# Kernel tuning notes

Hardware: AMD Instinct MI355X
Metric: run time of the kernel (lower is better)

The kernel has to match this reference:

```python
import jax, jax.numpy as jnp
import numpy as np

B, L, D = 4, 1024, 1024
N, H = 16, 64
FFW = 4096
LYR = 6
PDIM = 768            # 3 * 16^2
POS_EMB = 64
POOL_K = 4
EPS = 1e-6
BASE = 10000.0
GRID = 32             # 32x32 patch grid


def rms_norm(x, scale=None, eps=EPS):
    v = jnp.mean(jnp.square(x.astype(jnp.float32)), axis=-1, keepdims=True)
    y = (x.astype(jnp.float32) * jax.lax.rsqrt(v + eps)).astype(x.dtype)
    return y * scale if scale is not None else y


def _rope_half(x, pos, base):
    # x: [B, L, N, Hh]; pos: [B, L] int coords
    Hh = x.shape[-1]
    inv = 1.0 / (base ** (jnp.arange(Hh // 2, dtype=jnp.float32) / (Hh // 2)))
    ang = pos.astype(jnp.float32)[..., None] * inv          # [B, L, Hh/2]
    cos = jnp.cos(ang)[:, :, None, :]
    sin = jnp.sin(ang)[:, :, None, :]
    x1, x2 = jnp.split(x, 2, axis=-1)
    return jnp.concatenate([x1 * cos - x2 * sin, x2 * cos + x1 * sin], axis=-1)


def apply_2d_rope(x, px, py, base):
    # first half of head_dim rotated by x-coord, second half by y-coord
    xa, xb = jnp.split(x, 2, axis=-1)
    return jnp.concatenate([_rope_half(xa, px, base), _rope_half(xb, py, base)], axis=-1)


def setup_inputs() -> dict:
    key = jax.random.key(0)
    ks = jax.random.split(key, 12)
    pixel_values = jax.random.uniform(ks[0], (B, L, PDIM), dtype=jnp.float32)
    gx = jnp.arange(L, dtype=jnp.int32) % GRID
    gy = jnp.arange(L, dtype=jnp.int32) // GRID
    position_ids = jnp.broadcast_to(jnp.stack([gx, gy], -1), (B, L, 2))
    s = 0.02
    Win = jax.random.normal(ks[1], (PDIM, D), jnp.float32) * s
    pos_table = jax.random.normal(ks[2], (2, POS_EMB, D), jnp.float32) * s
    Wq = jax.random.normal(ks[3], (LYR, D, N * H), jnp.float32) * s
    Wk = jax.random.normal(ks[4], (LYR, D, N * H), jnp.float32) * s
    Wv = jax.random.normal(ks[5], (LYR, D, N * H), jnp.float32) * s
    Wo = jax.random.normal(ks[6], (LYR, N * H, D), jnp.float32) * s
    Wg = jax.random.normal(ks[7], (LYR, D, FFW), jnp.float32) * s
    Wu = jax.random.normal(ks[8], (LYR, D, FFW), jnp.float32) * s
    Wd = jax.random.normal(ks[9], (LYR, FFW, D), jnp.float32) * s
    qn = jnp.ones((LYR, H), jnp.float32)
    kn = jnp.ones((LYR, H), jnp.float32)
    pre_attn = jnp.ones((LYR, D), jnp.float32)
    post_attn = jnp.ones((LYR, D), jnp.float32)
    pre_ffw = jnp.ones((LYR, D), jnp.float32)
    post_ffw = jnp.ones((LYR, D), jnp.float32)
    return dict(pixel_values=pixel_values, position_ids=position_ids, Win=Win,
                pos_table=pos_table, Wq=Wq, Wk=Wk, Wv=Wv, Wo=Wo, qn=qn, kn=kn,
                pre_attn=pre_attn, post_attn=post_attn, pre_ffw=pre_ffw,
                post_ffw=post_ffw, Wg=Wg, Wu=Wu, Wd=Wd)


def _encoder(pixel_values, position_ids, Win, pos_table, Wq, Wk, Wv, Wo, qn, kn,
             pre_attn, post_attn, pre_ffw, post_ffw, Wg, Wu, Wd):
    padding = jnp.all(position_ids == -1, axis=-1)          # [B, L] True = pad
    valid = ~padding
    big_neg = jnp.finfo(jnp.float32).min
    amask = jnp.where((valid[:, :, None] & valid[:, None, :])[:, None], 0.0, big_neg)  # [B,1,L,L]

    px = position_ids[:, :, 0]
    py = position_ids[:, :, 1]
    clamped = jnp.maximum(position_ids, 0)

    # patch embed
    pix = 2.0 * (pixel_values - 0.5)
    x = pix @ Win
    pos_emb = pos_table[0][clamped[..., 0]] + pos_table[1][clamped[..., 1]]
    x = x + jnp.where(padding[..., None], 0.0, pos_emb)

    for i in range(LYR):
        # attention
        res = x
        h = rms_norm(x, pre_attn[i])
        q = (h @ Wq[i]).reshape(B, L, N, H)
        k = (h @ Wk[i]).reshape(B, L, N, H)
        v = (h @ Wv[i]).reshape(B, L, N, H)
        q = rms_norm(q, qn[i])
        k = rms_norm(k, kn[i])
        v = rms_norm(v)                                     # with_scale=False
        q = apply_2d_rope(q, px, py, BASE)
        k = apply_2d_rope(k, px, py, BASE)
        scores = jnp.einsum('bqnh,bknh->bnqk', q, k) + amask  # no 1/sqrt(H), matches source
        w = jax.nn.softmax(scores.astype(jnp.float32), axis=-1).astype(v.dtype)
        o = jnp.einsum('bnqk,bknh->bqnh', w, v).reshape(B, L, N * H) @ Wo[i]
        x = res + rms_norm(o, post_attn[i])
        # GeGLU MLP
        res = x
        h = rms_norm(x, pre_ffw[i])
        m = (jax.nn.gelu(h @ Wg[i], approximate=True) * (h @ Wu[i])) @ Wd[i]
        x = res + rms_norm(m, post_ffw[i])

    # pooler: 4x4 position-based average pooling
    out_len = L // (POOL_K ** 2)
    kk = int((L / out_len) ** 0.5)
    x = jnp.where(padding[..., None], 0.0, x)
    max_x = jnp.max(clamped[..., 0], axis=-1, keepdims=True) + 1   # [B,1]
    kidx = clamped // kk
    kidx = kidx[..., 0] + (max_x // kk) * kidx[..., 1]             # [B, L]
    weights = jax.nn.one_hot(kidx, out_len, dtype=jnp.float32) / (kk * kk)
    pooled = jnp.einsum('blo,bld->bod', weights, x.astype(jnp.float32))
    mask = jnp.any(weights != 0, axis=1)                           # [B, out_len]
    pooled = pooled.astype(x.dtype) * jnp.sqrt(jnp.float32(D))
    pooled = jnp.where(mask[..., None], pooled, 0.0)               # jit-safe stand-in for hidden[mask]
    return pooled, mask


def reference(pixel_values, position_ids, Win, pos_table, Wq, Wk, Wv, Wo, qn, kn,
              pre_attn, post_attn, pre_ffw, post_ffw, Wg, Wu, Wd):
    return _encoder(pixel_values, position_ids, Win, pos_table, Wq, Wk, Wv, Wo,
                    qn, kn, pre_attn, post_attn, pre_ffw, post_ffw, Wg, Wu, Wd)
```

## Files before the change

### kernel.cpp

```cpp
#include <hip/hip_runtime.h>
#include <stdint.h>

typedef unsigned short ushort_t;
using frag8 = __attribute__((ext_vector_type(8))) short;
using f32x4 = __attribute__((ext_vector_type(4))) float;

static __device__ __forceinline__ unsigned short f2bf(float f) {
  union { float f; unsigned u; } v; v.f = f;
  unsigned r = v.u + 0x7fffu + ((v.u >> 16) & 1u);
  return (unsigned short)(r >> 16);
}
static __device__ __forceinline__ float bf2f(unsigned short b) {
  union { unsigned u; float f; } v; v.u = ((unsigned)b) << 16; return v.f;
}
static __device__ __forceinline__ void splitf(float v, ushort_t& h, ushort_t& m) {
  h = f2bf(v);
  m = f2bf(v - bf2f(h));
}

__global__ __launch_bounds__(256) void k_splitpix(const float* __restrict__ pix,
                                                  ushort_t* __restrict__ oh,
                                                  ushort_t* __restrict__ om, int n4) {
  int i = blockIdx.x * 256 + threadIdx.x;
  if (i >= n4) return;
  float4 v = ((const float4*)pix)[i];
  ushort4 h, m;
  splitf(2.f * (v.x - 0.5f), h.x, m.x);
  splitf(2.f * (v.y - 0.5f), h.y, m.y);
  splitf(2.f * (v.z - 0.5f), h.z, m.z);
  splitf(2.f * (v.w - 0.5f), h.w, m.w);
  ((ushort4*)oh)[i] = h;
  ((ushort4*)om)[i] = m;
}

__global__ __launch_bounds__(256) void k_wsplit4(const float* __restrict__ B0,
                                                 const float* __restrict__ B1,
                                                 const float* __restrict__ B2,
                                                 const float* __restrict__ B3,
                                                 ushort_t* __restrict__ th,
                                                 ushort_t* __restrict__ tm,
                                                 int K, int N) {
  __shared__ float ts[64][65];
  const int z = blockIdx.z;
  const float* B = (z == 0) ? B0 : (z == 1) ? B1 : (z == 2) ? B2 : B3;
  th += (size_t)z * K * N;
  tm += (size_t)z * K * N;
  const int tid = threadIdx.x;
  const int n0 = blockIdx.x << 6, k0 = blockIdx.y << 6;
  int rr = tid >> 4, cc = (tid & 15) << 2;
#pragma unroll
  for (int j = 0; j < 4; ++j) {
    int r = rr + j * 16;
    float4 v = *(const float4*)(B + (size_t)(k0 + r) * N + n0 + cc);
    ts[r][cc] = v.x; ts[r][cc + 1] = v.y; ts[r][cc + 2] = v.z; ts[r][cc + 3] = v.w;
  }
  __syncthreads();
  int n = tid >> 2;
  int kc = (tid & 3) << 4;
  ushort_t oh[16], om[16];
#pragma unroll
  for (int j = 0; j < 16; ++j) splitf(ts[kc + j][n], oh[j], om[j]);
  ushort_t* ph = th + (size_t)(n0 + n) * K + k0 + kc;
  ushort_t* pm = tm + (size_t)(n0 + n) * K + k0 + kc;
  *(uint4*)(ph) = *(uint4*)(oh);
  *(uint4*)(ph + 8) = *(uint4*)(oh + 8);
  *(uint4*)(pm) = *(uint4*)(om);
  *(uint4*)(pm + 8) = *(uint4*)(om + 8);
}

__global__ __launch_bounds__(256) void k_posemb(const int* __restrict__ pos,
                                                const float* __restrict__ ptab,
                                                float* __restrict__ x) {
  int row = blockIdx.x, tid = threadIdx.x;
  int p0 = pos[(size_t)row * 2], p1 = pos[(size_t)row * 2 + 1];
  bool pad = (p0 == -1) && (p1 == -1);
  int px = p0 > 0 ? p0 : 0, py = p1 > 0 ? p1 : 0;
  float4 a = ((const float4*)(ptab + (size_t)px * 1024))[tid];
  float4 b = ((const float4*)(ptab + 65536 + (size_t)py * 1024))[tid];
  float4 o;
  o.x = pad ? 0.f : a.x + b.x;
  o.y = pad ? 0.f : a.y + b.y;
  o.z = pad ? 0.f : a.z + b.z;
  o.w = pad ? 0.f : a.w + b.w;
  ((float4*)(x + (size_t)row * 1024))[tid] = o;
}

__global__ __launch_bounds__(256) void k_rmsnorm_s(const float* __restrict__ x,
                                                   const float* __restrict__ scale,
                                                   ushort_t* __restrict__ oh,
                                                   ushort_t* __restrict__ om) {
  __shared__ float wsum[4];
  int row = blockIdx.x, tid = threadIdx.x;
  float4 v = ((const float4*)(x + (size_t)row * 1024))[tid];
  float ss = v.x * v.x + v.y * v.y + v.z * v.z + v.w * v.w;
  for (int m = 1; m < 64; m <<= 1) ss += __shfl_xor(ss, m);
  if ((tid & 63) == 0) wsum[tid >> 6] = ss;
  __syncthreads();
  float tot = wsum[0] + wsum[1] + wsum[2] + wsum[3];
  float r = rsqrtf(tot * (1.f / 1024.f) + 1e-6f);
  float4 sc = ((const float4*)scale)[tid];
  ushort4 h, m;
  splitf(v.x * r * sc.x, h.x, m.x);
  splitf(v.y * r * sc.y, h.y, m.y);
  splitf(v.z * r * sc.z, h.z, m.z);
  splitf(v.w * r * sc.w, h.w, m.w);
  ((ushort4*)(oh + (size_t)row * 1024))[tid] = h;
  ((ushort4*)(om + (size_t)row * 1024))[tid] = m;
}

__global__ __launch_bounds__(256) void k_addrms32(float* __restrict__ x,
                                                  const float* __restrict__ t,
                                                  const float* __restrict__ scale) {
  __shared__ float wsum[4];
  int row = blockIdx.x, tid = threadIdx.x;
  float4 v = ((const float4*)(t + (size_t)row * 1024))[tid];
  float ss = v.x * v.x + v.y * v.y + v.z * v.z + v.w * v.w;
  for (int m = 1; m < 64; m <<= 1) ss += __shfl_xor(ss, m);
  if ((tid & 63) == 0) wsum[tid >> 6] = ss;
  __syncthreads();
  float tot = wsum[0] + wsum[1] + wsum[2] + wsum[3];
  float r = rsqrtf(tot * (1.f / 1024.f) + 1e-6f);
  float4 sc = ((const float4*)scale)[tid];
  float4 xv = ((const float4*)(x + (size_t)row * 1024))[tid];
  xv.x += v.x * r * sc.x;
  xv.y += v.y * r * sc.y;
  xv.z += v.z * r * sc.z;
  xv.w += v.w * r * sc.w;
  ((float4*)(x + (size_t)row * 1024))[tid] = xv;
}

__global__ __launch_bounds__(256) void k_qkv(const ushort_t* __restrict__ Ah,
                                             const ushort_t* __restrict__ Am,
                                             const ushort_t* __restrict__ WT_h,
                                             const ushort_t* __restrict__ WT_m,
                                             const float* __restrict__ qn,
                                             const float* __restrict__ kn,
                                             const int* __restrict__ pos,
                                             ushort_t* __restrict__ qh, ushort_t* __restrict__ qm,
                                             ushort_t* __restrict__ kh, ushort_t* __restrict__ km,
                                             ushort_t* __restrict__ vh, ushort_t* __restrict__ vm) {
  __shared__ __align__(16) ushort_t Ash[128][40];
  __shared__ __align__(16) ushort_t Asl[128][40];
  __shared__ __align__(16) ushort_t Bsh[128][40];
  __shared__ __align__(16) ushort_t Bsl[128][40];
  const int tid = threadIdx.x;
  const int bid = blockIdx.x;
  const int xcd = bid & 7, lo = bid >> 3;
  const int ntl = lo % 3, mt = lo / 3;
  const int nt = xcd * 3 + ntl;
  const int mat = nt >> 3;
  const int n0 = (nt & 7) << 7;
  const int m0 = mt << 7;
  const ushort_t* Bh = WT_h + (size_t)mat * 1048576;
  const ushort_t* Bm = WT_m + (size_t)mat * 1048576;

  const int lane = tid & 63;
  const int wm = ((tid >> 7) & 1) * 64;
  const int wn = ((tid >> 6) & 1) * 64;
  const int l15 = lane & 15, lg = lane >> 4;
  const int srow = tid >> 1, scol = (tid & 1) << 4;
  f32x4 acc[4][4] = {};

  for (int k0 = 0; k0 < 1024; k0 += 32) {
    const ushort_t* gah = Ah + (size_t)(m0 + srow) * 1024 + k0 + scol;
    const ushort_t* gam = Am + (size_t)(m0 + srow) * 1024 + k0 + scol;
    const ushort_t* gbh = Bh + (size_t)(n0 + srow) * 1024 + k0 + scol;
    const ushort_t* gbm = Bm + (size_t)(n0 + srow) * 1024 + k0 + scol;
    uint4 a0 = *(const uint4*)gah, a1 = *(const uint4*)(gah + 8);
    uint4 a2 = *(const uint4*)gam, a3 = *(const uint4*)(gam + 8);
    uint4 b0 = *(const uint4*)gbh, b1 = *(const uint4*)(gbh + 8);
    uint4 b2 = *(const uint4*)gbm, b3 = *(const uint4*)(gbm + 8);
    *(uint4*)(&Ash[srow][scol]) = a0;
    *(uint4*)(&Ash[srow][scol + 8]) = a1;
    *(uint4*)(&Asl[srow][scol]) = a2;
    *(uint4*)(&Asl[srow][scol + 8]) = a3;
    *(uint4*)(&Bsh[srow][scol]) = b0;
    *(uint4*)(&Bsh[srow][scol + 8]) = b1;
    *(uint4*)(&Bsl[srow][scol]) = b2;
    *(uint4*)(&Bsl[srow][scol + 8]) = b3;
    __syncthreads();
    frag8 ah[4], al[4], bh[4], bl[4];
#pragma unroll
    for (int i = 0; i < 4; ++i) {
      ah[i] = *(const frag8*)(&Ash[wm + i * 16 + l15][lg << 3]);
      al[i] = *(const frag8*)(&Asl[wm + i * 16 + l15][lg << 3]);
      bh[i] = *(const frag8*)(&Bsh[wn + i * 16 + l15][lg << 3]);
      bl[i] = *(const frag8*)(&Bsl[wn + i * 16 + l15][lg << 3]);
    }
#pragma unroll
    for (int mi = 0; mi < 4; ++mi)
#pragma unroll
      for (int ni = 0; ni < 4; ++ni) {
        acc[mi][ni] = __builtin_amdgcn_mfma_f32_16x16x32_bf16(ah[mi], bh[ni], acc[mi][ni], 0, 0, 0);
        acc[mi][ni] = __builtin_amdgcn_mfma_f32_16x16x32_bf16(ah[mi], bl[ni], acc[mi][ni], 0, 0, 0);
        acc[mi][ni] = __builtin_amdgcn_mfma_f32_16x16x32_bf16(al[mi], bh[ni], acc[mi][ni], 0, 0, 0);
      }
    __syncthreads();
  }

  const float* scale = (mat == 0) ? qn : (mat == 1 ? kn : nullptr);
  ushort_t* outh = (mat == 0) ? qh : (mat == 1 ? kh : vh);
  ushort_t* outm = (mat == 0) ? qm : (mat == 1 ? km : vm);
  const float inv = powf(10000.f, -(float)l15 * (1.f / 16.f));
#pragma unroll
  for (int mi = 0; mi < 4; ++mi) {
#pragma unroll
    for (int rr = 0; rr < 4; ++rr) {
      float ss = 0.f;
#pragma unroll
      for (int ni = 0; ni < 4; ++ni) { float v = acc[mi][ni][rr]; ss += v * v; }
      ss += __shfl_xor(ss, 1);
      ss += __shfl_xor(ss, 2);
      ss += __shfl_xor(ss, 4);
      ss += __shfl_xor(ss, 8);
      float rs = rsqrtf(ss * (1.f / 64.f) + 1e-6f);
      int row = m0 + wm + mi * 16 + (lg << 2) + rr;
      float nv[4];
#pragma unroll
      for (int ni = 0; ni < 4; ++ni) {
        float sc = scale ? scale[ni * 16 + l15] : 1.f;
        nv[ni] = acc[mi][ni][rr] * rs * sc;
      }
      if (mat < 2) {
        int p0 = pos[(size_t)row * 2], p1 = pos[(size_t)row * 2 + 1];
        p0 = p0 > 0 ? p0 : 0;
        p1 = p1 > 0 ? p1 : 0;
        float a0 = (float)p0 * inv, a1 = (float)p1 * inv;
        float c0 = cosf(a0), s0 = sinf(a0);
        float c1 = cosf(a1), s1 = sinf(a1);
        float t0 = nv[0] * c0 - nv[1] * s0;
        float t1 = nv[1] * c0 + nv[0] * s0;
        float t2 = nv[2] * c1 - nv[3] * s1;
        float t3 = nv[3] * c1 + nv[2] * s1;
        nv[0] = t0; nv[1] = t1; nv[2] = t2; nv[3] = t3;
      }
#pragma unroll
      for (int ni = 0; ni < 4; ++ni) {
        ushort_t h, m;
        splitf(nv[ni], h, m);
        size_t idx = (size_t)row * 1024 + n0 + wn + ni * 16 + l15;
        outh[idx] = h;
        outm[idx] = m;
      }
    }
  }
}

__global__ __launch_bounds__(256) void k_ffw_up(const ushort_t* __restrict__ Ah,
                                                const ushort_t* __restrict__ Am,
                                                const ushort_t* __restrict__ Gh,
                                                const ushort_t* __restrict__ Gm,
                                                const ushort_t* __restrict__ Uh,
                                                const ushort_t* __restrict__ Um,
                                                ushort_t* __restrict__ Oh,
                                                ushort_t* __restrict__ Om) {
  __shared__ __align__(16) ushort_t Ash[128][40];
  __shared__ __align__(16) ushort_t Asl[128][40];
  __shared__ __align__(16) ushort_t Bgh[128][40];
  __shared__ __align__(16) ushort_t Bgl[128][40];
  __shared__ __align__(16) ushort_t Buh[128][40];
  __shared__ __align__(16) ushort_t Bul[128][40];
  const int tid = threadIdx.x;
  const int bid = blockIdx.x;
  const int xcd = bid & 7, lo = bid >> 3;
  const int nt = xcd * 4 + (lo & 3);
  const int mt = lo >> 2;
  const int m0 = mt << 7, n0 = nt << 7;
  const int lane = tid & 63;
  const int wm = ((tid >> 7) & 1) * 64;
  const int wn = ((tid >> 6) & 1) * 64;
  const int l15 = lane & 15, lg = lane >> 4;
  const int srow = tid >> 1, scol = (tid & 1) << 4;
  f32x4 ag[4][4] = {};
  f32x4 au[4][4] = {};

  for (int k0 = 0; k0 < 1024; k0 += 32) {
    const ushort_t* gah = Ah + (size_t)(m0 + srow) * 1024 + k0 + scol;
    const ushort_t* gam = Am + (size_t)(m0 + srow) * 1024 + k0 + scol;
    const ushort_t* ggh = Gh + (size_t)(n0 + srow) * 1024 + k0 + scol;
    const ushort_t* ggm = Gm + (size_t)(n0 + srow) * 1024 + k0 + scol;
    const ushort_t* guh = Uh + (size_t)(n0 + srow) * 1024 + k0 + scol;
    const ushort_t* gum = Um + (size_t)(n0 + srow) * 1024 + k0 + scol;
    uint4 a0 = *(const uint4*)gah, a1 = *(const uint4*)(gah + 8);
    uint4 a2 = *(const uint4*)gam, a3 = *(const uint4*)(gam + 8);
    uint4 g0 = *(const uint4*)ggh, g1 = *(const uint4*)(ggh + 8);
    uint4 g2 = *(const uint4*)ggm, g3 = *(const uint4*)(ggm + 8);
    uint4 u0 = *(const uint4*)guh, u1 = *(const uint4*)(guh + 8);
    uint4 u2 = *(const uint4*)gum, u3 = *(const uint4*)(gum + 8);
    *(uint4*)(&Ash[srow][scol]) = a0;
    *(uint4*)(&Ash[srow][scol + 8]) = a1;
    *(uint4*)(&Asl[srow][scol]) = a2;
    *(uint4*)(&Asl[srow][scol + 8]) = a3;
    *(uint4*)(&Bgh[srow][scol]) = g0;
    *(uint4*)(&Bgh[srow][scol + 8]) = g1;
    *(uint4*)(&Bgl[srow][scol]) = g2;
    *(uint4*)(&Bgl[srow][scol + 8]) = g3;
    *(uint4*)(&Buh[srow][scol]) = u0;
    *(uint4*)(&Buh[srow][scol + 8]) = u1;
    *(uint4*)(&Bul[srow][scol]) = u2;
    *(uint4*)(&Bul[srow][scol + 8]) = u3;
    __syncthreads();
    frag8 ah[4], al[4];
#pragma unroll
    for (int i = 0; i < 4; ++i) {
      ah[i] = *(const frag8*)(&Ash[wm + i * 16 + l15][lg << 3]);
      al[i] = *(const frag8*)(&Asl[wm + i * 16 + l15][lg << 3]);
    }
#pragma unroll
    for (int ni = 0; ni < 4; ++ni) {
      frag8 bgh = *(const frag8*)(&Bgh[wn + ni * 16 + l15][lg << 3]);
      frag8 bgl = *(const frag8*)(&Bgl[wn + ni * 16 + l15][lg << 3]);
      frag8 buh = *(const frag8*)(&Buh[wn + ni * 16 + l15][lg << 3]);
      frag8 bul = *(const frag8*)(&Bul[wn + ni * 16 + l15][lg << 3]);
#pragma unroll
      for (int mi = 0; mi < 4; ++mi) {
        ag[mi][ni] = __builtin_amdgcn_mfma_f32_16x16x32_bf16(ah[mi], bgh, ag[mi][ni], 0, 0, 0);
        ag[mi][ni] = __builtin_amdgcn_mfma_f32_16x16x32_bf16(ah[mi], bgl, ag[mi][ni], 0, 0, 0);
        ag[mi][ni] = __builtin_amdgcn_mfma_f32_16x16x32_bf16(al[mi], bgh, ag[mi][ni], 0, 0, 0);
        au[mi][ni] = __builtin_amdgcn_mfma_f32_16x16x32_bf16(ah[mi], buh, au[mi][ni], 0, 0, 0);
        au[mi][ni] = __builtin_amdgcn_mfma_f32_16x16x32_bf16(ah[mi], bul, au[mi][ni], 0, 0, 0);
        au[mi][ni] = __builtin_amdgcn_mfma_f32_16x16x32_bf16(al[mi], buh, au[mi][ni], 0, 0, 0);
      }
    }
    __syncthreads();
  }

#pragma unroll
  for (int mi = 0; mi < 4; ++mi) {
#pragma unroll
    for (int ni = 0; ni < 4; ++ni) {
#pragma unroll
      for (int r = 0; r < 4; ++r) {
        float vg = ag[mi][ni][r];
        float x3 = vg * vg * vg;
        float gel = 0.5f * vg * (1.f + tanhf(0.7978845608028654f * (vg + 0.044715f * x3)));
        float v2 = gel * au[mi][ni][r];
        int gr = m0 + wm + mi * 16 + (lg << 2) + r;
        int gc = n0 + wn + ni * 16 + l15;
        size_t idx = (size_t)gr * 4096 + gc;
        ushort_t h, m;
        splitf(v2, h, m);
        Oh[idx] = h;
        Om[idx] = m;
      }
    }
  }
}

enum { EPI_F32 = 0, EPI_ADDF32 = 1 };

template <int EPI>
__global__ __launch_bounds__(256) void k_gemm_s(const ushort_t* __restrict__ Ah,
                                                const ushort_t* __restrict__ Am,
                                                const ushort_t* __restrict__ Bh,
                                                const ushort_t* __restrict__ Bm,
                                                float* Cf, int K, int N) {
  __shared__ __align__(16) ushort_t Ash[128][40];
  __shared__ __align__(16) ushort_t Asl[128][40];
  __shared__ __align__(16) ushort_t Bsh[128][40];
  __shared__ __align__(16) ushort_t Bsl[128][40];
  const int tid = threadIdx.x;
  const int bid = blockIdx.x;
  const int xcd = bid & 7, lo = bid >> 3;
  const int mt = xcd * 4 + (lo >> 3);
  const int nt = lo & 7;
  const int m0 = mt << 7, n0 = nt << 7;
  const int lane = tid & 63;
  const int wm = ((tid >> 7) & 1) * 64;
  const int wn = ((tid >> 6) & 1) * 64;
  const int l15 = lane & 15, lg = lane >> 4;
  const int srow = tid >> 1, scol = (tid & 1) << 4;
  f32x4 acc[4][4] = {};

  for (int k0 = 0; k0 < K; k0 += 32) {
    const ushort_t* gah = Ah + (size_t)(m0 + srow) * K + k0 + scol;
    const ushort_t* gam = Am + (size_t)(m0 + srow) * K + k0 + scol;
    const ushort_t* gbh = Bh + (size_t)(n0 + srow) * K + k0 + scol;
    const ushort_t* gbm = Bm + (size_t)(n0 + srow) * K + k0 + scol;
    uint4 a0 = *(const uint4*)gah, a1 = *(const uint4*)(gah + 8);
    uint4 a2 = *(const uint4*)gam, a3 = *(const uint4*)(gam + 8);
    uint4 b0 = *(const uint4*)gbh, b1 = *(const uint4*)(gbh + 8);
    uint4 b2 = *(const uint4*)gbm, b3 = *(const uint4*)(gbm + 8);
    *(uint4*)(&Ash[srow][scol]) = a0;
    *(uint4*)(&Ash[srow][scol + 8]) = a1;
    *(uint4*)(&Asl[srow][scol]) = a2;
    *(uint4*)(&Asl[srow][scol + 8]) = a3;
    *(uint4*)(&Bsh[srow][scol]) = b0;
    *(uint4*)(&Bsh[srow][scol + 8]) = b1;
    *(uint4*)(&Bsl[srow][scol]) = b2;
    *(uint4*)(&Bsl[srow][scol + 8]) = b3;
    __syncthreads();
    frag8 ah[4], al[4], bh[4], bl[4];
#pragma unroll
    for (int i = 0; i < 4; ++i) {
      ah[i] = *(const frag8*)(&Ash[wm + i * 16 + l15][lg << 3]);
      al[i] = *(const frag8*)(&Asl[wm + i * 16 + l15][lg << 3]);
      bh[i] = *(const frag8*)(&Bsh[wn + i * 16 + l15][lg << 3]);
      bl[i] = *(const frag8*)(&Bsl[wn + i * 16 + l15][lg << 3]);
    }
#pragma unroll
    for (int mi = 0; mi < 4; ++mi)
#pragma unroll
      for (int ni = 0; ni < 4; ++ni) {
        acc[mi][ni] = __builtin_amdgcn_mfma_f32_16x16x32_bf16(ah[mi], bh[ni], acc[mi][ni], 0, 0, 0);
        acc[mi][ni] = __builtin_amdgcn_mfma_f32_16x16x32_bf16(ah[mi], bl[ni], acc[mi][ni], 0, 0, 0);
        acc[mi][ni] = __builtin_amdgcn_mfma_f32_16x16x32_bf16(al[mi], bh[ni], acc[mi][ni], 0, 0, 0);
      }
    __syncthreads();
  }

#pragma unroll
  for (int mi = 0; mi < 4; ++mi) {
#pragma unroll
    for (int ni = 0; ni < 4; ++ni) {
#pragma unroll
      for (int r = 0; r < 4; ++r) {
        float val = acc[mi][ni][r];
        int gr = m0 + wm + mi * 16 + (lg << 2) + r;
        int gc = n0 + wn + ni * 16 + l15;
        size_t idx = (size_t)gr * N + gc;
        if (EPI == EPI_F32) Cf[idx] = val;
        else Cf[idx] += val;
      }
    }
  }
}

__global__ __launch_bounds__(256) void k_attn_s(const ushort_t* __restrict__ qh,
                                                const ushort_t* __restrict__ qm,
                                                const ushort_t* __restrict__ kh,
                                                const ushort_t* __restrict__ km,
                                                const ushort_t* __restrict__ vh,
                                                const ushort_t* __restrict__ vm,
                                                ushort_t* __restrict__ oh,
                                                ushort_t* __restrict__ om) {
  __shared__ __align__(16) ushort_t Khs[64][72];
  __shared__ __align__(16) ushort_t Kms[64][72];
  __shared__ __align__(16) ushort_t Vhs[64][72];
  __shared__ __align__(16) ushort_t Vms[64][72];
  __shared__ __align__(16) ushort_t Phs[64][72];
  __shared__ __align__(16) ushort_t Pms[64][72];
  const int tid = threadIdx.x;
  const int bid = blockIdx.x;
  const int xcd = bid & 7, lo = bid >> 3;
  const int bh_ = xcd * 8 + (lo >> 4);
  const int qt = lo & 15;
  const int b = bh_ >> 4, n = bh_ & 15;
  const size_t base = (size_t)b * 1048576 + (size_t)n * 64;
  const int lane = tid & 63, w = tid >> 6;
  const int l15 = lane & 15, lg = lane >> 4;

  {
    int row = tid >> 2, cg = (tid & 3) << 4;
    const uint4* sh = (const uint4*)(qh + base + (size_t)(qt * 64 + row) * 1024 + cg);
    const uint4* sm = (const uint4*)(qm + base + (size_t)(qt * 64 + row) * 1024 + cg);
    uint4 h0 = sh[0], h1 = sh[1], m0v = sm[0], m1v = sm[1];
    *(uint4*)(&Khs[row][cg]) = h0;
    *(uint4*)(&Khs[row][cg + 8]) = h1;
    *(uint4*)(&Kms[row][cg]) = m0v;
    *(uint4*)(&Kms[row][cg + 8]) = m1v;
  }
  __syncthreads();
  frag8 qh0 = *(const frag8*)(&Khs[w * 16 + l15][lg << 3]);
  frag8 qh1 = *(const frag8*)(&Khs[w * 16 + l15][32 + (lg << 3)]);
  frag8 qm0 = *(const frag8*)(&Kms[w * 16 + l15][lg << 3]);
  frag8 qm1 = *(const frag8*)(&Kms[w * 16 + l15][32 + (lg << 3)]);

  f32x4 oacc[4] = {};
  float mrun[4], srun[4];
#pragma unroll
  for (int r = 0; r < 4; ++r) { mrun[r] = -3.0e38f; srun[r] = 0.f; }

  for (int t = 0; t < 16; ++t) {
    __syncthreads();
    {
      int row = tid >> 2, cg = (tid & 3) << 4;
      const uint4* sh = (const uint4*)(kh + base + (size_t)(t * 64 + row) * 1024 + cg);
      const uint4* sm = (const uint4*)(km + base + (size_t)(t * 64 + row) * 1024 + cg);
      uint4 h0 = sh[0], h1 = sh[1], m0v = sm[0], m1v = sm[1];
      *(uint4*)(&Khs[row][cg]) = h0;
      *(uint4*)(&Khs[row][cg + 8]) = h1;
      *(uint4*)(&Kms[row][cg]) = m0v;
      *(uint4*)(&Kms[row][cg + 8]) = m1v;
    }
    {
      int hcol = tid & 63, kg = tid >> 6;
      ushort_t th[16], tm_[16];
#pragma unroll
      for (int j = 0; j < 16; ++j) {
        size_t off = base + (size_t)(t * 64 + kg * 16 + j) * 1024 + hcol;
        th[j] = vh[off];
        tm_[j] = vm[off];
      }
#pragma unroll
      for (int g = 0; g < 4; ++g) {
        ushort4 wv, wv2;
        wv.x = th[g * 4]; wv.y = th[g * 4 + 1]; wv.z = th[g * 4 + 2]; wv.w = th[g * 4 + 3];
        wv2.x = tm_[g * 4]; wv2.y = tm_[g * 4 + 1]; wv2.z = tm_[g * 4 + 2]; wv2.w = tm_[g * 4 + 3];
        *(ushort4*)(&Vhs[hcol][kg * 16 + g * 4]) = wv;
        *(ushort4*)(&Vms[hcol][kg * 16 + g * 4]) = wv2;
      }
    }
    __syncthreads();

    f32x4 sacc[4] = {};
#pragma unroll
    for (int nf = 0; nf < 4; ++nf) {
      frag8 kh0 = *(const frag8*)(&Khs[nf * 16 + l15][lg << 3]);
      frag8 kh1 = *(const frag8*)(&Khs[nf * 16 + l15][32 + (lg << 3)]);
      frag8 km0 = *(const frag8*)(&Kms[nf * 16 + l15][lg << 3]);
      frag8 km1 = *(const frag8*)(&Kms[nf * 16 + l15][32 + (lg << 3)]);
      sacc[nf] = __builtin_amdgcn_mfma_f32_16x16x32_bf16(qh0, kh0, sacc[nf], 0, 0, 0);
      sacc[nf] = __builtin_amdgcn_mfma_f32_16x16x32_bf16(qh1, kh1, sacc[nf], 0, 0, 0);
      sacc[nf] = __builtin_amdgcn_mfma_f32_16x16x32_bf16(qh0, km0, sacc[nf], 0, 0, 0);
      sacc[nf] = __builtin_amdgcn_mfma_f32_16x16x32_bf16(qh1, km1, sacc[nf], 0, 0, 0);
      sacc[nf] = __builtin_amdgcn_mfma_f32_16x16x32_bf16(qm0, kh0, sacc[nf], 0, 0, 0);
      sacc[nf] = __builtin_amdgcn_mfma_f32_16x16x32_bf16(qm1, kh1, sacc[nf], 0, 0, 0);
    }
#pragma unroll
    for (int r = 0; r < 4; ++r) {
      float tm = fmaxf(fmaxf(sacc[0][r], sacc[1][r]), fmaxf(sacc[2][r], sacc[3][r]));
      tm = fmaxf(tm, __shfl_xor(tm, 1));
      tm = fmaxf(tm, __shfl_xor(tm, 2));
      tm = fmaxf(tm, __shfl_xor(tm, 4));
      tm = fmaxf(tm, __shfl_xor(tm, 8));
      float nm = fmaxf(mrun[r], tm);
      float al = expf(mrun[r] - nm);
      float p0 = expf(sacc[0][r] - nm);
      float p1 = expf(sacc[1][r] - nm);
      float p2 = expf(sacc[2][r] - nm);
      float p3 = expf(sacc[3][r] - nm);
      float rs = p0 + p1 + p2 + p3;
      rs += __shfl_xor(rs, 1);
      rs += __shfl_xor(rs, 2);
      rs += __shfl_xor(rs, 4);
      rs += __shfl_xor(rs, 8);
      srun[r] = srun[r] * al + rs;
      mrun[r] = nm;
#pragma unroll
      for (int hf = 0; hf < 4; ++hf) oacc[hf][r] *= al;
      int prow = w * 16 + lg * 4 + r;
      ushort_t ph, pm;
      splitf(p0, ph, pm); Phs[prow][0 * 16 + l15] = ph; Pms[prow][0 * 16 + l15] = pm;
      splitf(p1, ph, pm); Phs[prow][1 * 16 + l15] = ph; Pms[prow][1 * 16 + l15] = pm;
      splitf(p2, ph, pm); Phs[prow][2 * 16 + l15] = ph; Pms[prow][2 * 16 + l15] = pm;
      splitf(p3, ph, pm); Phs[prow][3 * 16 + l15] = ph; Pms[prow][3 * 16 + l15] = pm;
    }
    __syncthreads();
#pragma unroll
    for (int kg = 0; kg < 2; ++kg) {
      frag8 pf = *(const frag8*)(&Phs[w * 16 + l15][kg * 32 + (lg << 3)]);
      frag8 pf2 = *(const frag8*)(&Pms[w * 16 + l15][kg * 32 + (lg << 3)]);
#pragma unroll
      for (int hf = 0; hf < 4; ++hf) {
        frag8 vf = *(const frag8*)(&Vhs[hf * 16 + l15][kg * 32 + (lg << 3)]);
        frag8 vf2 = *(const frag8*)(&Vms[hf * 16 + l15][kg * 32 + (lg << 3)]);
        oacc[hf] = __builtin_amdgcn_mfma_f32_16x16x32_bf16(pf, vf, oacc[hf], 0, 0, 0);
        oacc[hf] = __builtin_amdgcn_mfma_f32_16x16x32_bf16(pf, vf2, oacc[hf], 0, 0, 0);
        oacc[hf] = __builtin_amdgcn_mfma_f32_16x16x32_bf16(pf2, vf, oacc[hf], 0, 0, 0);
      }
    }
  }
#pragma unroll
  for (int hf = 0; hf < 4; ++hf)
#pragma unroll
    for (int r = 0; r < 4; ++r) {
      float val = oacc[hf][r] / srun[r];
      size_t off = base + (size_t)(qt * 64 + w * 16 + lg * 4 + r) * 1024 + hf * 16 + l15;
      ushort_t h, m;
      splitf(val, h, m);
      oh[off] = h;
      om[off] = m;
    }
}

__global__ __launch_bounds__(256) void k_pool(const float* __restrict__ x,
                                              const int* __restrict__ pos,
                                              float* __restrict__ out,
                                              float* __restrict__ maskout) {
  __shared__ int smax[4];
  __shared__ int kidx_s[1024];
  const int blk = blockIdx.x;
  const int b = blk >> 6, oidx = blk & 63;
  const int tid = threadIdx.x;
  int mx = 0;
  for (int l = tid; l < 1024; l += 256) {
    int p0 = pos[((size_t)b * 1024 + l) * 2];
    mx = max(mx, p0 > 0 ? p0 : 0);
  }
  for (int m = 1; m < 64; m <<= 1) mx = max(mx, __shfl_xor(mx, m));
  if ((tid & 63) == 0) smax[tid >> 6] = mx;
  __syncthreads();
  int maxx = max(max(smax[0], smax[1]), max(smax[2], smax[3])) + 1;
  int mk = maxx >> 2;
  for (int l = tid; l < 1024; l += 256) {
    int p0 = pos[((size_t)b * 1024 + l) * 2];
    int p1 = pos[((size_t)b * 1024 + l) * 2 + 1];
    int c0 = p0 > 0 ? p0 : 0, c1 = p1 > 0 ? p1 : 0;
    int pad = (p0 == -1 && p1 == -1) ? 1 : 0;
    kidx_s[l] = ((c0 >> 2) + mk * (c1 >> 2)) | (pad << 16);
  }
  __syncthreads();
  float ax = 0.f, ay = 0.f, az = 0.f, aw = 0.f;
  int cnt = 0;
  for (int l = 0; l < 1024; ++l) {
    int ki = kidx_s[l];
    if ((ki & 0xffff) == oidx) {
      cnt++;
      if (!(ki >> 16)) {
        float4 xv = ((const float4*)(x + ((size_t)b * 1024 + l) * 1024))[tid];
        ax += xv.x; ay += xv.y; az += xv.z; aw += xv.w;
      }
    }
  }
  float4 res;
  res.x = ax * 2.0f; res.y = ay * 2.0f; res.z = az * 2.0f; res.w = aw * 2.0f;
  ((float4*)(out + ((size_t)b * 64 + oidx) * 1024))[tid] = res;
  if (tid == 0) maskout[b * 64 + oidx] = (cnt > 0) ? 1.0f : 0.0f;
}

extern "C" void kernel_launch(void* const* d_in, const int* in_sizes, int n_in,
                              void* d_out, int out_size, void* d_ws, size_t ws_size,
                              hipStream_t stream) {
  const float* pix = (const float*)d_in[0];
  const int* pos = (const int*)d_in[1];
  const float* Win = (const float*)d_in[2];
  const float* ptab = (const float*)d_in[3];
  const float* Wq = (const float*)d_in[4];
  const float* Wk = (const float*)d_in[5];
  const float* Wv = (const float*)d_in[6];
  const float* Wo = (const float*)d_in[7];
  const float* qn = (const float*)d_in[8];
  const float* kn = (const float*)d_in[9];
  const float* pre_attn = (const float*)d_in[10];
  const float* post_attn = (const float*)d_in[11];
  const float* pre_ffw = (const float*)d_in[12];
  const float* post_ffw = (const float*)d_in[13];
  const float* Wg = (const float*)d_in[14];
  const float* Wu = (const float*)d_in[15];
  const float* Wd = (const float*)d_in[16];

  char* w = (char*)d_ws;
  float* x = (float*)w;        w += 16777216;
  float* tmp = (float*)w;      w += 16777216;
  ushort_t* hh = (ushort_t*)w; w += 8388608;
  ushort_t* hm = (ushort_t*)w; w += 8388608;
  char* regB = w;
  ushort_t* qh_ = (ushort_t*)(regB + 0);
  ushort_t* qm_ = (ushort_t*)(regB + 8388608);
  ushort_t* kh_ = (ushort_t*)(regB + 16777216);
  ushort_t* km_ = (ushort_t*)(regB + 25165824);
  ushort_t* vh_ = (ushort_t*)(regB + 33554432);
  ushort_t* vm_ = (ushort_t*)(regB + 41943040);
  ushort_t* aoh = (ushort_t*)(regB + 50331648);
  ushort_t* aom = (ushort_t*)(regB + 58720256);
  ushort_t* wat_h = (ushort_t*)(regB + 67108864);
  ushort_t* wat_m = (ushort_t*)(regB + 75497472);
  ushort_t* mh = (ushort_t*)(regB + 0);
  ushort_t* mm = (ushort_t*)(regB + 33554432);
  ushort_t* wgu_h = (ushort_t*)(regB + 67108864);
  ushort_t* wgu_m = (ushort_t*)(regB + 83886080);
  ushort_t* wd_h = (ushort_t*)(regB + 100663296);
  ushort_t* wd_m = (ushort_t*)(regB + 109051904);
  ushort_t* pixh = (ushort_t*)(regB + 0);
  ushort_t* pixm = (ushort_t*)(regB + 6291456);
  ushort_t* win_h = (ushort_t*)(regB + 67108864);
  ushort_t* win_m = (ushort_t*)(regB + 71303168);

  dim3 blk(256);
  k_splitpix<<<3072, blk, 0, stream>>>(pix, pixh, pixm, 786432);
  k_posemb<<<4096, blk, 0, stream>>>(pos, ptab, x);
  k_wsplit4<<<dim3(16, 12, 1), blk, 0, stream>>>(Win, Win, Win, Win, win_h, win_m, 768, 1024);
  k_gemm_s<EPI_ADDF32><<<256, blk, 0, stream>>>(pixh, pixm, win_h, win_m, x, 768, 1024);

  for (int i = 0; i < 6; ++i) {
    const float* wq = Wq + (size_t)i * 1048576;
    const float* wk = Wk + (size_t)i * 1048576;
    const float* wv = Wv + (size_t)i * 1048576;
    const float* wo = Wo + (size_t)i * 1048576;
    const float* wg = Wg + (size_t)i * 4194304;
    const float* wu = Wu + (size_t)i * 4194304;
    const float* wd = Wd + (size_t)i * 4194304;

    k_rmsnorm_s<<<4096, blk, 0, stream>>>(x, pre_attn + i * 1024, hh, hm);
    k_wsplit4<<<dim3(16, 16, 4), blk, 0, stream>>>(wq, wk, wv, wo, wat_h, wat_m, 1024, 1024);
    k_qkv<<<768, blk, 0, stream>>>(hh, hm, wat_h, wat_m, qn + i * 64, kn + i * 64, pos,
                                   qh_, qm_, kh_, km_, vh_, vm_);
    k_attn_s<<<1024, blk, 0, stream>>>(qh_, qm_, kh_, km_, vh_, vm_, aoh, aom);
    k_gemm_s<EPI_F32><<<256, blk, 0, stream>>>(aoh, aom, wat_h + 3145728, wat_m + 3145728,
                                               tmp, 1024, 1024);
    k_addrms32<<<4096, blk, 0, stream>>>(x, tmp, post_attn + i * 1024);

    k_rmsnorm_s<<<4096, blk, 0, stream>>>(x, pre_ffw + i * 1024, hh, hm);
    k_wsplit4<<<dim3(64, 16, 2), blk, 0, stream>>>(wg, wu, wg, wu, wgu_h, wgu_m, 1024, 4096);
    k_wsplit4<<<dim3(16, 64, 1), blk, 0, stream>>>(wd, wd, wd, wd, wd_h, wd_m, 4096, 1024);
    k_ffw_up<<<1024, blk, 0, stream>>>(hh, hm, wgu_h, wgu_m, wgu_h + 4194304, wgu_m + 4194304,
                                       mh, mm);
    k_gemm_s<EPI_F32><<<256, blk, 0, stream>>>(mh, mm, wd_h, wd_m, tmp, 4096, 1024);
    k_addrms32<<<4096, blk, 0, stream>>>(x, tmp, post_ffw + i * 1024);
  }

  k_pool<<<256, blk, 0, stream>>>(x, pos, (float*)d_out, (float*)d_out + 262144);
}
```

Baseline: 5.186 ms.

## Split-K the output-projection and down GEMMs and swizzle LDS tile columns

The attention output-projection and FFN down-projection GEMMs are split into two K-halves. This doubles the grid from 256 to 512 blocks, and each half writes its own fp32 partial buffer into workspace freed by earlier stages. The add+RMSNorm kernel now sums the two partials before normalizing, so no separate reduction kernel is needed. All MFMA GEMM kernels also XOR-swizzle the 8-element column chunks in shared memory to cut LDS bank conflicts on the fragment reads. The cost is extra partial-sum memory traffic and reuse of aliased workspace regions.

```diff
diff --git a/kernel.cpp b/kernel.cpp
--- a/kernel.cpp
+++ b/kernel.cpp
@@ -109,11 +109,14 @@
 }
 
 __global__ __launch_bounds__(256) void k_addrms32(float* __restrict__ x,
-                                                  const float* __restrict__ t,
+                                                  const float* __restrict__ t1,
+                                                  const float* __restrict__ t2,
                                                   const float* __restrict__ scale) {
   __shared__ float wsum[4];
   int row = blockIdx.x, tid = threadIdx.x;
-  float4 v = ((const float4*)(t + (size_t)row * 1024))[tid];
+  float4 v = ((const float4*)(t1 + (size_t)row * 1024))[tid];
+  float4 v2 = ((const float4*)(t2 + (size_t)row * 1024))[tid];
+  v.x += v2.x; v.y += v2.y; v.z += v2.z; v.w += v2.w;
   float ss = v.x * v.x + v.y * v.y + v.z * v.z + v.w * v.w;
   for (int m = 1; m < 64; m <<= 1) ss += __shfl_xor(ss, m);
   if ((tid & 63) == 0) wsum[tid >> 6] = ss;
@@ -128,6 +131,8 @@
   xv.w += v.w * r * sc.w;
   ((float4*)(x + (size_t)row * 1024))[tid] = xv;
 }
+
+#define SWZ_COL(r, c) (((c) ^ (((r) >> 3) & 3)) << 3)
 
 __global__ __launch_bounds__(256) void k_qkv(const ushort_t* __restrict__ Ah,
                                              const ushort_t* __restrict__ Am,
@@ -159,6 +164,8 @@
   const int wn = ((tid >> 6) & 1) * 64;
   const int l15 = lane & 15, lg = lane >> 4;
   const int srow = tid >> 1, scol = (tid & 1) << 4;
+  const int cb = (tid & 1) << 1;
+  const int wc0 = SWZ_COL(srow, cb), wc1 = SWZ_COL(srow, cb + 1);
   f32x4 acc[4][4] = {};
 
   for (int k0 = 0; k0 < 1024; k0 += 32) {
@@ -170,22 +177,24 @@
     uint4 a2 = *(const uint4*)gam, a3 = *(const uint4*)(gam + 8);
     uint4 b0 = *(const uint4*)gbh, b1 = *(const uint4*)(gbh + 8);
     uint4 b2 = *(const uint4*)gbm, b3 = *(const uint4*)(gbm + 8);
-    *(uint4*)(&Ash[srow][scol]) = a0;
-    *(uint4*)(&Ash[srow][scol + 8]) = a1;
-    *(uint4*)(&Asl[srow][scol]) = a2;
-    *(uint4*)(&Asl[srow][scol + 8]) = a3;
-    *(uint4*)(&Bsh[srow][scol]) = b0;
-    *(uint4*)(&Bsh[srow][scol + 8]) = b1;
-    *(uint4*)(&Bsl[srow][scol]) = b2;
-    *(uint4*)(&Bsl[srow][scol + 8]) = b3;
+    *(uint4*)(&Ash[srow][wc0]) = a0;
+    *(uint4*)(&Ash[srow][wc1]) = a1;
+    *(uint4*)(&Asl[srow][wc0]) = a2;
+    *(uint4*)(&Asl[srow][wc1]) = a3;
+    *(uint4*)(&Bsh[srow][wc0]) = b0;
+    *(uint4*)(&Bsh[srow][wc1]) = b1;
+    *(uint4*)(&Bsl[srow][wc0]) = b2;
+    *(uint4*)(&Bsl[srow][wc1]) = b3;
     __syncthreads();
     frag8 ah[4], al[4], bh[4], bl[4];
 #pragma unroll
     for (int i = 0; i < 4; ++i) {
-      ah[i] = *(const frag8*)(&Ash[wm + i * 16 + l15][lg << 3]);
-      al[i] = *(const frag8*)(&Asl[wm + i * 16 + l15][lg << 3]);
-      bh[i] = *(const frag8*)(&Bsh[wn + i * 16 + l15][lg << 3]);
-      bl[i] = *(const frag8*)(&Bsl[wn + i * 16 + l15][lg << 3]);
+      int rA = wm + i * 16 + l15, rB = wn + i * 16 + l15;
+      int cA = SWZ_COL(rA, lg), cB = SWZ_COL(rB, lg);
+      ah[i] = *(const frag8*)(&Ash[rA][cA]);
+      al[i] = *(const frag8*)(&Asl[rA][cA]);
+      bh[i] = *(const frag8*)(&Bsh[rB][cB]);
+      bl[i] = *(const frag8*)(&Bsl[rB][cB]);
     }
 #pragma unroll
     for (int mi = 0; mi < 4; ++mi)
@@ -271,6 +280,8 @@
   const int wn = ((tid >> 6) & 1) * 64;
   const int l15 = lane & 15, lg = lane >> 4;
   const int srow = tid >> 1, scol = (tid & 1) << 4;
+  const int cb = (tid & 1) << 1;
+  const int wc0 = SWZ_COL(srow, cb), wc1 = SWZ_COL(srow, cb + 1);
   f32x4 ag[4][4] = {};
   f32x4 au[4][4] = {};
 
@@ -287,31 +298,35 @@
     uint4 g2 = *(const uint4*)ggm, g3 = *(const uint4*)(ggm + 8);
     uint4 u0 = *(const uint4*)guh, u1 = *(const uint4*)(guh + 8);
     uint4 u2 = *(const uint4*)gum, u3 = *(const uint4*)(gum + 8);
-    *(uint4*)(&Ash[srow][scol]) = a0;
-    *(uint4*)(&Ash[srow][scol + 8]) = a1;
-    *(uint4*)(&Asl[srow][scol]) = a2;
-    *(uint4*)(&Asl[srow][scol + 8]) = a3;
-    *(uint4*)(&Bgh[srow][scol]) = g0;
-    *(uint4*)(&Bgh[srow][scol + 8]) = g1;
-    *(uint4*)(&Bgl[srow][scol]) = g2;
-    *(uint4*)(&Bgl[srow][scol + 8]) = g3;
-    *(uint4*)(&Buh[srow][scol]) = u0;
-    *(uint4*)(&Buh[srow][scol + 8]) = u1;
-    *(uint4*)(&Bul[srow][scol]) = u2;
-    *(uint4*)(&Bul[srow][scol + 8]) = u3;
+    *(uint4*)(&Ash[srow][wc0]) = a0;
+    *(uint4*)(&Ash[srow][wc1]) = a1;
+    *(uint4*)(&Asl[srow][wc0]) = a2;
+    *(uint4*)(&Asl[srow][wc1]) = a3;
+    *(uint4*)(&Bgh[srow][wc0]) = g0;
+    *(uint4*)(&Bgh[srow][wc1]) = g1;
+    *(uint4*)(&Bgl[srow][wc0]) = g2;
+    *(uint4*)(&Bgl[srow][wc1]) = g3;
+    *(uint4*)(&Buh[srow][wc0]) = u0;
+    *(uint4*)(&Buh[srow][wc1]) = u1;
+    *(uint4*)(&Bul[srow][wc0]) = u2;
+    *(uint4*)(&Bul[srow][wc1]) = u3;
     __syncthreads();
     frag8 ah[4], al[4];
 #pragma unroll
     for (int i = 0; i < 4; ++i) {
-      ah[i] = *(const frag8*)(&Ash[wm + i * 16 + l15][lg << 3]);
-      al[i] = *(const frag8*)(&Asl[wm + i * 16 + l15][lg << 3]);
+      int rA = wm + i * 16 + l15;
+      int cA = SWZ_COL(rA, lg);
+      ah[i] = *(const frag8*)(&Ash[rA][cA]);
+      al[i] = *(const frag8*)(&Asl[rA][cA]);
     }
 #pragma unroll
     for (int ni = 0; ni < 4; ++ni) {
-      frag8 bgh = *(const frag8*)(&Bgh[wn + ni * 16 + l15][lg << 3]);
-      frag8 bgl = *(const frag8*)(&Bgl[wn + ni * 16 + l15][lg << 3]);
-      frag8 buh = *(const frag8*)(&Buh[wn + ni * 16 + l15][lg << 3]);
-      frag8 bul = *(const frag8*)(&Bul[wn + ni * 16 + l15][lg << 3]);
+      int rB = wn + ni * 16 + l15;
+      int cB = SWZ_COL(rB, lg);
+      frag8 bgh = *(const frag8*)(&Bgh[rB][cB]);
+      frag8 bgl = *(const frag8*)(&Bgl[rB][cB]);
+      frag8 buh = *(const frag8*)(&Buh[rB][cB]);
+      frag8 bul = *(const frag8*)(&Bul[rB][cB]);
 #pragma unroll
       for (int mi = 0; mi < 4; ++mi) {
         ag[mi][ni] = __builtin_amdgcn_mfma_f32_16x16x32_bf16(ah[mi], bgh, ag[mi][ni], 0, 0, 0);
@@ -354,14 +369,19 @@
                                                 const ushort_t* __restrict__ Am,
                                                 const ushort_t* __restrict__ Bh,
                                                 const ushort_t* __restrict__ Bm,
-                                                float* Cf, int K, int N) {
+                                                float* C0, float* C1,
+                                                int K, int N, int ksteps) {
   __shared__ __align__(16) ushort_t Ash[128][40];
   __shared__ __align__(16) ushort_t Asl[128][40];
   __shared__ __align__(16) ushort_t Bsh[128][40];
   __shared__ __align__(16) ushort_t Bsl[128][40];
   const int tid = threadIdx.x;
   const int bid = blockIdx.x;
-  const int xcd = bid & 7, lo = bid >> 3;
+  const int half = bid >> 8;
+  const int inner = bid & 255;
+  float* Cf = half ? C1 : C0;
+  const int kbase = half * ksteps * 32;
+  const int xcd = inner & 7, lo = inner >> 3;
   const int mt = xcd * 4 + (lo >> 3);
   const int nt = lo & 7;
   const int m0 = mt << 7, n0 = nt << 7;
@@ -370,9 +390,12 @@
   const int wn = ((tid >> 6) & 1) * 64;
   const int l15 = lane & 15, lg = lane >> 4;
   const int srow = tid >> 1, scol = (tid & 1) << 4;
+  const int cb = (tid & 1) << 1;
+  const int wc0 = SWZ_COL(srow, cb), wc1 = SWZ_COL(srow, cb + 1);
   f32x4 acc[4][4] = {};
 
-  for (int k0 = 0; k0 < K; k0 += 32) {
+  for (int ks = 0; ks < ksteps; ++ks) {
+    const int k0 = kbase + ks * 32;
     const ushort_t* gah = Ah + (size_t)(m0 + srow) * K + k0 + scol;
     const ushort_t* gam = Am + (size_t)(m0 + srow) * K + k0 + scol;
     const ushort_t* gbh = Bh + (size_t)(n0 + srow) * K + k0 + scol;
@@ -381,22 +404,24 @@
     uint4 a2 = *(const uint4*)gam, a3 = *(const uint4*)(gam + 8);
     uint4 b0 = *(const uint4*)gbh, b1 = *(const uint4*)(gbh + 8);
     uint4 b2 = *(const uint4*)gbm, b3 = *(const uint4*)(gbm + 8);
-    *(uint4*)(&Ash[srow][scol]) = a0;
-    *(uint4*)(&Ash[srow][scol + 8]) = a1;
-    *(uint4*)(&Asl[srow][scol]) = a2;
-    *(uint4*)(&Asl[srow][scol + 8]) = a3;
-    *(uint4*)(&Bsh[srow][scol]) = b0;
-    *(uint4*)(&Bsh[srow][scol + 8]) = b1;
-    *(uint4*)(&Bsl[srow][scol]) = b2;
-    *(uint4*)(&Bsl[srow][scol + 8]) = b3;
+    *(uint4*)(&Ash[srow][wc0]) = a0;
+    *(uint4*)(&Ash[srow][wc1]) = a1;
+    *(uint4*)(&Asl[srow][wc0]) = a2;
+    *(uint4*)(&Asl[srow][wc1]) = a3;
+    *(uint4*)(&Bsh[srow][wc0]) = b0;
+    *(uint4*)(&Bsh[srow][wc1]) = b1;
+    *(uint4*)(&Bsl[srow][wc0]) = b2;
+    *(uint4*)(&Bsl[srow][wc1]) = b3;
     __syncthreads();
     frag8 ah[4], al[4], bh[4], bl[4];
 #pragma unroll
     for (int i = 0; i < 4; ++i) {
-      ah[i] = *(const frag8*)(&Ash[wm + i * 16 + l15][lg << 3]);
-      al[i] = *(const frag8*)(&Asl[wm + i * 16 + l15][lg << 3]);
-      bh[i] = *(const frag8*)(&Bsh[wn + i * 16 + l15][lg << 3]);
-      bl[i] = *(const frag8*)(&Bsl[wn + i * 16 + l15][lg << 3]);
+      int rA = wm + i * 16 + l15, rB = wn + i * 16 + l15;
+      int cA = SWZ_COL(rA, lg), cB = SWZ_COL(rB, lg);
+      ah[i] = *(const frag8*)(&Ash[rA][cA]);
+      al[i] = *(const frag8*)(&Asl[rA][cA]);
+      bh[i] = *(const frag8*)(&Bsh[rB][cB]);
+      bl[i] = *(const frag8*)(&Bsl[rB][cB]);
     }
 #pragma unroll
     for (int mi = 0; mi < 4; ++mi)
@@ -656,12 +681,14 @@
   ushort_t* aom = (ushort_t*)(regB + 58720256);
   ushort_t* wat_h = (ushort_t*)(regB + 67108864);
   ushort_t* wat_m = (ushort_t*)(regB + 75497472);
+  float* t2o = (float*)(regB + 0);
   ushort_t* mh = (ushort_t*)(regB + 0);
   ushort_t* mm = (ushort_t*)(regB + 33554432);
   ushort_t* wgu_h = (ushort_t*)(regB + 67108864);
   ushort_t* wgu_m = (ushort_t*)(regB + 83886080);
   ushort_t* wd_h = (ushort_t*)(regB + 100663296);
   ushort_t* wd_m = (ushort_t*)(regB + 109051904);
+  float* t2d = (float*)(regB + 67108864);
   ushort_t* pixh = (ushort_t*)(regB + 0);
   ushort_t* pixm = (ushort_t*)(regB + 6291456);
   ushort_t* win_h = (ushort_t*)(regB + 67108864);
@@ -671,7 +698,8 @@
   k_splitpix<<<3072, blk, 0, stream>>>(pix, pixh, pixm, 786432);
   k_posemb<<<4096, blk, 0, stream>>>(pos, ptab, x);
   k_wsplit4<<<dim3(16, 12, 1), blk, 0, stream>>>(Win, Win, Win, Win, win_h, win_m, 768, 1024);
-  k_gemm_s<EPI_ADDF32><<<256, blk, 0, stream>>>(pixh, pixm, win_h, win_m, x, 768, 1024);
+  k_gemm_s<EPI_ADDF32><<<256, blk, 0, stream>>>(pixh, pixm, win_h, win_m, x, nullptr,
+                                                768, 1024, 24);
 
   for (int i = 0; i < 6; ++i) {
     const float* wq = Wq + (size_t)i * 1048576;
@@ -687,17 +715,17 @@
     k_qkv<<<768, blk, 0, stream>>>(hh, hm, wat_h, wat_m, qn + i * 64, kn + i * 64, pos,
                                    qh_, qm_, kh_, km_, vh_, vm_);
     k_attn_s<<<1024, blk, 0, stream>>>(qh_, qm_, kh_, km_, vh_, vm_, aoh, aom);
-    k_gemm_s<EPI_F32><<<256, blk, 0, stream>>>(aoh, aom, wat_h + 3145728, wat_m + 3145728,
-                                               tmp, 1024, 1024);
-    k_addrms32<<<4096, blk, 0, stream>>>(x, tmp, post_attn + i * 1024);
+    k_gemm_s<EPI_F32><<<512, blk, 0, stream>>>(aoh, aom, wat_h + 3145728, wat_m + 3145728,
+                                               tmp, t2o, 1024, 1024, 16);
+    k_addrms32<<<4096, blk, 0, stream>>>(x, tmp, t2o, post_attn + i * 1024);
 
     k_rmsnorm_s<<<4096, blk, 0, stream>>>(x, pre_ffw + i * 1024, hh, hm);
     k_wsplit4<<<dim3(64, 16, 2), blk, 0, stream>>>(wg, wu, wg, wu, wgu_h, wgu_m, 1024, 4096);
     k_wsplit4<<<dim3(16, 64, 1), blk, 0, stream>>>(wd, wd, wd, wd, wd_h, wd_m, 4096, 1024);
     k_ffw_up<<<1024, blk, 0, stream>>>(hh, hm, wgu_h, wgu_m, wgu_h + 4194304, wgu_m + 4194304,
                                        mh, mm);
-    k_gemm_s<EPI_F32><<<256, blk, 0, stream>>>(mh, mm, wd_h, wd_m, tmp, 4096, 1024);
-    k_addrms32<<<4096, blk, 0, stream>>>(x, tmp, post_ffw + i * 1024);
+    k_gemm_s<EPI_F32><<<512, blk, 0, stream>>>(mh, mm, wd_h, wd_m, tmp, t2d, 4096, 1024, 64);
+    k_addrms32<<<4096, blk, 0, stream>>>(x, tmp, t2d, post_ffw + i * 1024);
   }
 
   k_pool<<<256, blk, 0, stream>>>(x, pos, (float*)d_out, (float*)d_out + 262144);
```

Measured after the change: 4.636 ms. 1.12x faster.
